# Kernel tuning notes

Measured on AMD Instinct MI355X. Metric: run time of the kernel, lower is better.

Reference implementation:

```python
import jax, jax.numpy as jnp
import numpy as np

N = 50000      # nodes
E = 800000     # edges (before self-loops)
IN = 128       # in_channels
HID = 64       # hidden_channels (= per-head dim, concat=False)
H = 4          # heads
OUT = 40       # out_channels
L = 4          # num_layers
LN_EPS = 1e-5


def setup_inputs() -> dict:
    key = jax.random.key(0)
    ks = jax.random.split(key, 12)
    s = 0.05
    return {
        "x": jax.random.normal(ks[0], (N, IN), jnp.float32),
        "edge_index": jax.random.randint(ks[1], (2, E), 0, N, dtype=jnp.int32),
        "Wi": jax.random.normal(ks[2], (IN, HID), jnp.float32) * s,
        "bi": jnp.zeros((HID,), jnp.float32),
        "lin_W": jax.random.normal(ks[3], (L, HID, H * HID), jnp.float32) * s,
        "att_src": jax.random.normal(ks[4], (L, H, HID), jnp.float32) * s,
        "att_dst": jax.random.normal(ks[5], (L, H, HID), jnp.float32) * s,
        "gat_b": jnp.zeros((L, HID), jnp.float32),
        "ln_g": jnp.ones((L, HID), jnp.float32),
        "ln_b": jnp.zeros((L, HID), jnp.float32),
        "Wo": jax.random.normal(ks[6], (HID, OUT), jnp.float32) * s,
        "bo": jnp.zeros((OUT,), jnp.float32),
    }


def _layer_norm(x, g, b):
    mu = jnp.mean(x, axis=-1, keepdims=True)
    var = jnp.mean(jnp.square(x - mu), axis=-1, keepdims=True)
    return (x - mu) * jax.lax.rsqrt(var + LN_EPS) * g + b


def _gat_conv(x, src, dst, W, a_src, a_dst, bias):
    # PyG GATConv: heads=H, out_channels=HID, concat=False (mean over heads),
    # negative_slope=0.2, self-loops already appended to (src, dst).
    xl = (x @ W).reshape(N, H, HID)                    # [N,H,C]
    alpha_s = jnp.einsum('nhc,hc->nh', xl, a_src)      # [N,H]
    alpha_d = jnp.einsum('nhc,hc->nh', xl, a_dst)      # [N,H]
    e = jax.nn.leaky_relu(alpha_s[src] + alpha_d[dst], 0.2)  # [Etot,H]
    # segment softmax over incoming edges of each destination node
    m = jax.ops.segment_max(e, dst, num_segments=N)    # [N,H]
    e = jnp.exp(e - m[dst])
    denom = jax.ops.segment_sum(e, dst, num_segments=N)
    alpha = e / (denom[dst] + 1e-16)                   # [Etot,H]
    msg = alpha[:, :, None] * xl[src]                  # [Etot,H,C]
    out = jax.ops.segment_sum(msg, dst, num_segments=N)  # [N,H,C]
    return out.mean(axis=1) + bias                     # concat=False -> mean


def reference(x, edge_index, Wi, bi, lin_W, att_src, att_dst, gat_b, ln_g, ln_b, Wo, bo):
    # add self-loops (GATConv default add_self_loops=True)
    loops = jnp.arange(N, dtype=edge_index.dtype)
    src = jnp.concatenate([edge_index[0], loops])
    dst = jnp.concatenate([edge_index[1], loops])

    h = jax.nn.elu(x @ Wi + bi)
    for i in range(L):
        residual = h
        h = _gat_conv(h, src, dst, lin_W[i], att_src[i], att_dst[i], gat_b[i])
        h = _layer_norm(h, ln_g[i], ln_b[i])
        h = jax.nn.elu(h)
        if i > 0:
            h = h + residual
        # dropout p=0.0 -> identity
    return h @ Wo + bo
```

## Files before the change

kernel.cpp:

```cpp
#include <hip/hip_runtime.h>
#include <hip/hip_bf16.h>

#define N_NODES 50000
#define N_EDGES 800000
#define E_TOT   (N_EDGES + N_NODES)
#define IN_CH   128
#define HID     64
#define HEADS   4
#define OUT_CH  40
#define LAYERS  4
#define LN_EPS  1e-5f

#define AG_STRIDE  262
#define WC_STRIDE  68

__device__ __forceinline__ unsigned short f2bf(float f) {
    unsigned u = __float_as_uint(f);
    unsigned r = (u + 0x7fffu + ((u >> 16) & 1u)) >> 16;
    return (unsigned short)r;
}
__device__ __forceinline__ float bf_lo(unsigned u) { return __uint_as_float(u << 16); }
__device__ __forceinline__ float bf_hi(unsigned u) { return __uint_as_float(u & 0xffff0000u); }
__device__ __forceinline__ float lrelu(float x) { return x > 0.f ? x : 0.2f * x; }

__device__ __forceinline__ unsigned fenc(float f) {
    unsigned u = __float_as_uint(f);
    return (u & 0x80000000u) ? ~u : (u | 0x80000000u);
}
__device__ __forceinline__ float fdec(unsigned k) {
    unsigned u = (k & 0x80000000u) ? (k & 0x7fffffffu) : ~k;
    return __uint_as_float(u);
}


__global__ void k_hist(const int* __restrict__ ei, int* __restrict__ cnt,
                       int* __restrict__ rank) {
    int e = blockIdx.x * blockDim.x + threadIdx.x;
    if (e >= E_TOT) return;
    int dst = (e < N_EDGES) ? ei[N_EDGES + e] : (e - N_EDGES);
    rank[e] = atomicAdd(&cnt[dst], 1);
}

__global__ __launch_bounds__(1024) void k_scan_a(const int* __restrict__ cnt,
                                                 int* __restrict__ row_ptr,
                                                 int* __restrict__ bsum) {
    __shared__ int wt[16];
    int tid = threadIdx.x, lane = tid & 63, w = tid >> 6;
    int i = blockIdx.x * 1024 + tid;
    int v = (i < N_NODES) ? cnt[i] : 0;
    int x = v;
    for (int off = 1; off < 64; off <<= 1) {
        int t = __shfl_up(x, off, 64);
        if (lane >= off) x += t;
    }
    if (lane == 63) wt[w] = x;
    __syncthreads();
    if (w == 0) {
        int t = (lane < 16) ? wt[lane] : 0;
        for (int off = 1; off < 16; off <<= 1) {
            int u = __shfl_up(t, off, 64);
            if (lane >= off) t += u;
        }
        if (lane < 16) wt[lane] = t;
    }
    __syncthreads();
    int woff = (w > 0) ? wt[w - 1] : 0;
    if (i < N_NODES) row_ptr[i] = woff + x - v;
    if (tid == 0) bsum[blockIdx.x] = wt[15];
}

#define SCAN_BLOCKS 49

__global__ __launch_bounds__(64) void k_scan_b(const int* __restrict__ bsum,
                                               int* __restrict__ boff,
                                               int* __restrict__ row_ptr) {
    int lane = threadIdx.x;
    int v = (lane < SCAN_BLOCKS) ? bsum[lane] : 0;
    int x = v;
    for (int off = 1; off < 64; off <<= 1) {
        int t = __shfl_up(x, off, 64);
        if (lane >= off) x += t;
    }
    if (lane < SCAN_BLOCKS) boff[lane] = x - v;
    if (lane == 63) row_ptr[N_NODES] = x;
}

__global__ __launch_bounds__(256) void k_scan_c(int* __restrict__ row_ptr,
                                                const int* __restrict__ boff) {
    int i = blockIdx.x * 256 + threadIdx.x;
    if (i >= N_NODES) return;
    row_ptr[i] += boff[i >> 10];
}

__global__ void k_scatter(const int* __restrict__ ei,
                          const int* __restrict__ row_ptr,
                          const int* __restrict__ rank,
                          int* __restrict__ csr_src) {
    int e = blockIdx.x * blockDim.x + threadIdx.x;
    if (e >= E_TOT) return;
    int src, dst;
    if (e < N_EDGES) { src = ei[e]; dst = ei[N_EDGES + e]; }
    else             { src = dst = e - N_EDGES; }
    int pos = row_ptr[dst] + rank[e];
    csr_src[pos] = src;
}


__global__ __launch_bounds__(256) void k_prep(const float* __restrict__ lin_W,
                                              const float* __restrict__ att_src,
                                              const float* __restrict__ att_dst,
                                              float* __restrict__ watt,
                                              float* __restrict__ wstack) {
    int l = blockIdx.x, tid = threadIdx.x;
    const float* Wl = lin_W + (size_t)l * HID * 256;
    {
        int k = tid, h = k >> 6, i = k & 63;
        const float* src = Wl + i * 256 + h * 64;
        float* dstp = wstack + (size_t)l * 256 * 64 + k * 64;
        for (int c = 0; c < 64; c += 4)
            *(float4*)(dstp + c) = *(const float4*)(src + c);
    }
    for (int idx = tid; idx < 512; idx += 256) {
        int v = idx >> 6, i = idx & 63;
        int h = v & 3;
        const float* av = (v < 4 ? att_src : att_dst) + (size_t)l * 256 + h * 64;
        const float* wr = Wl + i * 256 + h * 64;
        float p = 0.f;
        for (int c = 0; c < 64; ++c) p = fmaf(wr[c], av[c], p);
        watt[(size_t)l * 512 + v * 64 + i] = p;
    }
}


__global__ __launch_bounds__(256) void k_gemm_in(const float* __restrict__ x,
                                                 const float* __restrict__ Wi,
                                                 const float* __restrict__ bi,
                                                 const float* __restrict__ watt,
                                                 float* __restrict__ h,
                                                 unsigned short* __restrict__ h_bf,
                                                 float* __restrict__ alpha_s,
                                                 float* __restrict__ alpha_d,
                                                 unsigned* __restrict__ mxk) {
    __shared__ float xT[IN_CH * 64];
    __shared__ float Ws[IN_CH * HID];
    __shared__ float wl[512];
    __shared__ unsigned s_mx[4];
    int tid = threadIdx.x;
    int row0 = blockIdx.x * 64;
    if (tid < 4) s_mx[tid] = 0;
    for (int i = tid; i < 512; i += 256) wl[i] = watt[i];
    for (int i = tid * 4; i < IN_CH * HID; i += 1024)
        *(float4*)(Ws + i) = *(const float4*)(Wi + i);
    {
        int r = tid >> 2, k0 = (tid & 3) * 32;
        int rr = row0 + r;
#pragma unroll
        for (int j = 0; j < 32; j += 4) {
            float4 v = (rr < N_NODES) ? *(const float4*)(x + (size_t)rr * IN_CH + k0 + j)
                                      : make_float4(0.f, 0.f, 0.f, 0.f);
            xT[(k0 + j    ) * 64 + r] = v.x;
            xT[(k0 + j + 1) * 64 + r] = v.y;
            xT[(k0 + j + 2) * 64 + r] = v.z;
            xT[(k0 + j + 3) * 64 + r] = v.w;
        }
    }
    __syncthreads();
    int tx = tid & 15, ty = tid >> 4;
    int c0 = tx * 4, r0 = ty * 4;
    float acc[4][4] = {};
    for (int k = 0; k < IN_CH; ++k) {
        float4 xv = *(const float4*)(xT + k * 64 + r0);
        float4 wv = *(const float4*)(Ws + k * HID + c0);
        float xr[4] = {xv.x, xv.y, xv.z, xv.w};
        float wc[4] = {wv.x, wv.y, wv.z, wv.w};
#pragma unroll
        for (int r = 0; r < 4; ++r)
#pragma unroll
            for (int c = 0; c < 4; ++c)
                acc[r][c] = fmaf(xr[r], wc[c], acc[r][c]);
    }
    float4 bv = *(const float4*)(bi + c0);
    float bcs[4] = {bv.x, bv.y, bv.z, bv.w};
    float rpmax[4] = {-1e30f, -1e30f, -1e30f, -1e30f};
#pragma unroll
    for (int r = 0; r < 4; ++r) {
        int rr = row0 + r0 + r;
        float vv[4];
#pragma unroll
        for (int c = 0; c < 4; ++c) {
            float t = acc[r][c] + bcs[c];
            vv[c] = t > 0.f ? t : (__expf(t) - 1.f);
        }
        if (rr < N_NODES) {
            *(float4*)(h + (size_t)rr * HID + c0) = make_float4(vv[0], vv[1], vv[2], vv[3]);
            unsigned short t4[4] = {f2bf(vv[0]), f2bf(vv[1]), f2bf(vv[2]), f2bf(vv[3])};
            *(uint2*)(h_bf + (size_t)rr * HID + c0) = *(uint2*)t4;
        }
        float red[8];
#pragma unroll
        for (int v = 0; v < 8; ++v) {
            const float* wv = wl + v * 64 + c0;
            float p = vv[0]*wv[0] + vv[1]*wv[1] + vv[2]*wv[2] + vv[3]*wv[3];
            p += __shfl_xor(p, 1, 64);
            p += __shfl_xor(p, 2, 64);
            p += __shfl_xor(p, 4, 64);
            p += __shfl_xor(p, 8, 64);
            red[v] = p;
        }
        if (tx == 0 && rr < N_NODES) {
            *(float4*)(alpha_s + (size_t)rr * 4) = make_float4(red[0], red[1], red[2], red[3]);
            *(float4*)(alpha_d + (size_t)rr * 4) = make_float4(red[4], red[5], red[6], red[7]);
#pragma unroll
            for (int hh = 0; hh < 4; ++hh) rpmax[hh] = fmaxf(rpmax[hh], red[hh]);
        }
    }
    if (tx == 0) {
#pragma unroll
        for (int hh = 0; hh < 4; ++hh) atomicMax(&s_mx[hh], fenc(rpmax[hh]));
    }
    __syncthreads();
    if (tid < 4) atomicMax(&mxk[tid], s_mx[tid]);
}


__global__ __launch_bounds__(256) void k_layer(
    const unsigned short* __restrict__ h_bf,
    const float* __restrict__ alpha_s,
    const float* __restrict__ alpha_d,
    const int* __restrict__ row_ptr,
    const int* __restrict__ csr_src,
    const unsigned* __restrict__ mxk,
    const float* __restrict__ wstack,
    const float* __restrict__ gat_b,
    const float* __restrict__ ln_g,
    const float* __restrict__ ln_b,
    const float* __restrict__ h_res,
    const float* __restrict__ watt_next,
    float* __restrict__ h_out,
    unsigned short* __restrict__ hbf_out,
    float* __restrict__ alpha_s_nxt,
    float* __restrict__ alpha_d_nxt,
    unsigned* __restrict__ mxk_next,
    int use_res, int do_alpha)
{
    __shared__ unsigned short aS[32 * AG_STRIDE];
    __shared__ float Wc[32 * WC_STRIDE];
    __shared__ unsigned s_mx[4];
    int tid = threadIdx.x;
    int row0 = blockIdx.x * 32;
    if (tid < 4) s_mx[tid] = 0;

    {
        int dl = tid >> 3, q = tid & 7;
        int d = row0 + dl;
        unsigned short* arow = aS + dl * AG_STRIDE + (q << 3);
        if (d < N_NODES) {
            int start = row_ptr[d], end = row_ptr[d + 1];
            float4 ad = *(const float4*)(alpha_d + (size_t)d * 4);
            float mp0 = lrelu(fdec(mxk[0]) + ad.x);
            float mp1 = lrelu(fdec(mxk[1]) + ad.y);
            float mp2 = lrelu(fdec(mxk[2]) + ad.z);
            float mp3 = lrelu(fdec(mxk[3]) + ad.w);

            float acc[4][8] = {};
            float ds0 = 0.f, ds1 = 0.f, ds2 = 0.f, ds3 = 0.f;

            int s = csr_src[start];
            float4 as = *(const float4*)(alpha_s + (size_t)s * 4);
            uint4  u  = *(const uint4*)(h_bf + ((size_t)s << 6) + (q << 3));

            for (int e = start; e < end; ++e) {
                int sn = (e + 1 < end) ? csr_src[e + 1] : 0;
                float4 as_n = *(const float4*)(alpha_s + (size_t)sn * 4);
                uint4  u_n  = *(const uint4*)(h_bf + ((size_t)sn << 6) + (q << 3));

                float w0 = __expf(lrelu(as.x + ad.x) - mp0);
                float w1 = __expf(lrelu(as.y + ad.y) - mp1);
                float w2 = __expf(lrelu(as.z + ad.z) - mp2);
                float w3 = __expf(lrelu(as.w + ad.w) - mp3);
                ds0 += w0; ds1 += w1; ds2 += w2; ds3 += w3;
                float f0 = bf_lo(u.x), f1 = bf_hi(u.x), f2 = bf_lo(u.y), f3 = bf_hi(u.y);
                float f4 = bf_lo(u.z), f5 = bf_hi(u.z), f6 = bf_lo(u.w), f7 = bf_hi(u.w);
                acc[0][0] = fmaf(w0, f0, acc[0][0]); acc[0][1] = fmaf(w0, f1, acc[0][1]);
                acc[0][2] = fmaf(w0, f2, acc[0][2]); acc[0][3] = fmaf(w0, f3, acc[0][3]);
                acc[0][4] = fmaf(w0, f4, acc[0][4]); acc[0][5] = fmaf(w0, f5, acc[0][5]);
                acc[0][6] = fmaf(w0, f6, acc[0][6]); acc[0][7] = fmaf(w0, f7, acc[0][7]);
                acc[1][0] = fmaf(w1, f0, acc[1][0]); acc[1][1] = fmaf(w1, f1, acc[1][1]);
                acc[1][2] = fmaf(w1, f2, acc[1][2]); acc[1][3] = fmaf(w1, f3, acc[1][3]);
                acc[1][4] = fmaf(w1, f4, acc[1][4]); acc[1][5] = fmaf(w1, f5, acc[1][5]);
                acc[1][6] = fmaf(w1, f6, acc[1][6]); acc[1][7] = fmaf(w1, f7, acc[1][7]);
                acc[2][0] = fmaf(w2, f0, acc[2][0]); acc[2][1] = fmaf(w2, f1, acc[2][1]);
                acc[2][2] = fmaf(w2, f2, acc[2][2]); acc[2][3] = fmaf(w2, f3, acc[2][3]);
                acc[2][4] = fmaf(w2, f4, acc[2][4]); acc[2][5] = fmaf(w2, f5, acc[2][5]);
                acc[2][6] = fmaf(w2, f6, acc[2][6]); acc[2][7] = fmaf(w2, f7, acc[2][7]);
                acc[3][0] = fmaf(w3, f0, acc[3][0]); acc[3][1] = fmaf(w3, f1, acc[3][1]);
                acc[3][2] = fmaf(w3, f2, acc[3][2]); acc[3][3] = fmaf(w3, f3, acc[3][3]);
                acc[3][4] = fmaf(w3, f4, acc[3][4]); acc[3][5] = fmaf(w3, f5, acc[3][5]);
                acc[3][6] = fmaf(w3, f6, acc[3][6]); acc[3][7] = fmaf(w3, f7, acc[3][7]);

                as = as_n; u = u_n; s = sn;
            }

            float inv[4] = {1.f / (ds0 + 1e-16f), 1.f / (ds1 + 1e-16f),
                            1.f / (ds2 + 1e-16f), 1.f / (ds3 + 1e-16f)};
#pragma unroll
            for (int hh = 0; hh < 4; ++hh) {
                unsigned short t8[8];
#pragma unroll
                for (int k = 0; k < 8; ++k) t8[k] = f2bf(acc[hh][k] * inv[hh]);
                *(uint4*)(arow + hh * 64) = *(uint4*)t8;
            }
        } else {
            uint4 z = make_uint4(0, 0, 0, 0);
#pragma unroll
            for (int hh = 0; hh < 4; ++hh) *(uint4*)(arow + hh * 64) = z;
        }
    }

    int tx = tid & 15, ty = tid >> 4;
    int c0 = tx * 4, r0 = ty * 2;
    float acc[2][4] = {};

    int wk = tid >> 3;
    int wc8 = (tid & 7) * 8;
    for (int chunk = 0; chunk < 8; ++chunk) {
        __syncthreads();
        {
            const float* wsrc = wstack + (size_t)(chunk * 32 + wk) * 64 + wc8;
            float* wdst = Wc + wk * WC_STRIDE + wc8;
            *(float4*)(wdst)     = *(const float4*)(wsrc);
            *(float4*)(wdst + 4) = *(const float4*)(wsrc + 4);
        }
        __syncthreads();
        int kbase = chunk * 32;
#pragma unroll
        for (int kb = 0; kb < 8; ++kb) {
            int kl = kb * 4;
            float4 w0 = *(const float4*)(Wc + (kl + 0) * WC_STRIDE + c0);
            float4 w1 = *(const float4*)(Wc + (kl + 1) * WC_STRIDE + c0);
            float4 w2 = *(const float4*)(Wc + (kl + 2) * WC_STRIDE + c0);
            float4 w3 = *(const float4*)(Wc + (kl + 3) * WC_STRIDE + c0);
#pragma unroll
            for (int r = 0; r < 2; ++r) {
                uint2 au = *(const uint2*)(aS + (r0 + r) * AG_STRIDE + kbase + kl);
                float a0 = bf_lo(au.x), a1 = bf_hi(au.x), a2 = bf_lo(au.y), a3 = bf_hi(au.y);
                acc[r][0] = fmaf(a0, w0.x, fmaf(a1, w1.x, fmaf(a2, w2.x, fmaf(a3, w3.x, acc[r][0]))));
                acc[r][1] = fmaf(a0, w0.y, fmaf(a1, w1.y, fmaf(a2, w2.y, fmaf(a3, w3.y, acc[r][1]))));
                acc[r][2] = fmaf(a0, w0.z, fmaf(a1, w1.z, fmaf(a2, w2.z, fmaf(a3, w3.z, acc[r][2]))));
                acc[r][3] = fmaf(a0, w0.w, fmaf(a1, w1.w, fmaf(a2, w2.w, fmaf(a3, w3.w, acc[r][3]))));
            }
        }
    }

    float4 gb = *(const float4*)(gat_b + c0);
    float bias[4] = {gb.x, gb.y, gb.z, gb.w};
    float4 lg = *(const float4*)(ln_g + c0);
    float4 lb = *(const float4*)(ln_b + c0);
    float gg[4] = {lg.x, lg.y, lg.z, lg.w};
    float bb[4] = {lb.x, lb.y, lb.z, lb.w};
    float rpmax[4] = {-1e30f, -1e30f, -1e30f, -1e30f};
#pragma unroll
    for (int r = 0; r < 2; ++r) {
        int rr = row0 + r0 + r;
        float o[4];
#pragma unroll
        for (int c = 0; c < 4; ++c) o[c] = acc[r][c] * 0.25f + bias[c];
        float s = o[0] + o[1] + o[2] + o[3];
        float s2 = o[0]*o[0] + o[1]*o[1] + o[2]*o[2] + o[3]*o[3];
        for (int off = 1; off < 16; off <<= 1) {
            s  += __shfl_xor(s,  off, 64);
            s2 += __shfl_xor(s2, off, 64);
        }
        float mu = s * (1.f / 64.f);
        float var = s2 * (1.f / 64.f) - mu * mu;
        float rstd = rsqrtf(var + LN_EPS);
        float vv[4];
#pragma unroll
        for (int c = 0; c < 4; ++c) {
            float t = (o[c] - mu) * rstd * gg[c] + bb[c];
            vv[c] = t > 0.f ? t : (__expf(t) - 1.f);
        }
        if (rr < N_NODES) {
            if (use_res) {
                float4 rv = *(const float4*)(h_res + (size_t)rr * HID + c0);
                vv[0] += rv.x; vv[1] += rv.y; vv[2] += rv.z; vv[3] += rv.w;
            }
            *(float4*)(h_out + (size_t)rr * HID + c0) = make_float4(vv[0], vv[1], vv[2], vv[3]);
            unsigned short t4[4] = {f2bf(vv[0]), f2bf(vv[1]), f2bf(vv[2]), f2bf(vv[3])};
            *(uint2*)(hbf_out + (size_t)rr * HID + c0) = *(uint2*)t4;
        }
        if (do_alpha) {
            float red[8];
#pragma unroll
            for (int v = 0; v < 8; ++v) {
                const float* wv = watt_next + v * 64 + c0;
                float p = vv[0]*wv[0] + vv[1]*wv[1] + vv[2]*wv[2] + vv[3]*wv[3];
                p += __shfl_xor(p, 1, 64);
                p += __shfl_xor(p, 2, 64);
                p += __shfl_xor(p, 4, 64);
                p += __shfl_xor(p, 8, 64);
                red[v] = p;
            }
            if (tx == 0 && rr < N_NODES) {
                *(float4*)(alpha_s_nxt + (size_t)rr * 4) = make_float4(red[0], red[1], red[2], red[3]);
                *(float4*)(alpha_d_nxt + (size_t)rr * 4) = make_float4(red[4], red[5], red[6], red[7]);
#pragma unroll
                for (int hh = 0; hh < 4; ++hh) rpmax[hh] = fmaxf(rpmax[hh], red[hh]);
            }
        }
    }
    if (do_alpha) {
        if (tx == 0) {
#pragma unroll
            for (int hh = 0; hh < 4; ++hh) atomicMax(&s_mx[hh], fenc(rpmax[hh]));
        }
        __syncthreads();
        if (tid < 4) atomicMax(&mxk_next[tid], s_mx[tid]);
    }
}


__global__ __launch_bounds__(256) void k_gemm_out(const float* __restrict__ h,
                                                  const float* __restrict__ Wo,
                                                  const float* __restrict__ bo,
                                                  float* __restrict__ out) {
    __shared__ float Ws[HID * OUT_CH];
    __shared__ float hs[6 * HID];
    int tid = threadIdx.x;
    int row0 = blockIdx.x * 6;
    for (int i = tid; i < HID * OUT_CH; i += 256) Ws[i] = Wo[i];
    for (int i = tid; i < 6 * HID; i += 256) {
        int r = row0 + (i >> 6);
        hs[i] = (r < N_NODES) ? h[(size_t)r * HID + (i & 63)] : 0.f;
    }
    __syncthreads();
    if (tid < 240) {
        int r = tid / 40, o = tid - r * 40;
        int rr = row0 + r;
        if (rr < N_NODES) {
            float acc = bo[o];
            for (int k = 0; k < HID; ++k)
                acc = fmaf(hs[r * HID + k], Ws[k * OUT_CH + o], acc);
            out[(size_t)row0 * OUT_CH + tid] = acc;
        }
    }
}


extern "C" void kernel_launch(void* const* d_in, const int* in_sizes, int n_in,
                              void* d_out, int out_size, void* d_ws, size_t ws_size,
                              hipStream_t stream) {
    const float* x       = (const float*)d_in[0];
    const int*   ei      = (const int*)  d_in[1];
    const float* Wi      = (const float*)d_in[2];
    const float* bi      = (const float*)d_in[3];
    const float* lin_W   = (const float*)d_in[4];
    const float* att_src = (const float*)d_in[5];
    const float* att_dst = (const float*)d_in[6];
    const float* gat_b   = (const float*)d_in[7];
    const float* ln_g    = (const float*)d_in[8];
    const float* ln_b    = (const float*)d_in[9];
    const float* Wo      = (const float*)d_in[10];
    const float* bo      = (const float*)d_in[11];
    float* out = (float*)d_out;

    char* ws = (char*)d_ws;
    size_t off = 0;
    auto alloc = [&](size_t bytes) -> void* {
        void* p = ws + off;
        off += (bytes + 255) & ~(size_t)255;
        return p;
    };
    float*          h_a      = (float*)alloc((size_t)N_NODES * HID * 4);
    float*          h_b      = (float*)alloc((size_t)N_NODES * HID * 4);
    unsigned short* hbf_a    = (unsigned short*)alloc((size_t)N_NODES * HID * 2);
    unsigned short* hbf_b    = (unsigned short*)alloc((size_t)N_NODES * HID * 2);
    float*          als_a    = (float*)alloc((size_t)N_NODES * 4 * 4);
    float*          ald_a    = (float*)alloc((size_t)N_NODES * 4 * 4);
    float*          als_b    = (float*)alloc((size_t)N_NODES * 4 * 4);
    float*          ald_b    = (float*)alloc((size_t)N_NODES * 4 * 4);
    int*            cnt      = (int*)  alloc((size_t)N_NODES * 4);
    int*            row_ptr  = (int*)  alloc((size_t)(N_NODES + 1) * 4);
    int*            csr_src  = (int*)  alloc((size_t)E_TOT * 4);
    int*            rank     = (int*)  alloc((size_t)E_TOT * 4);
    unsigned*       maxkey   = (unsigned*)alloc((size_t)LAYERS * 4 * 4);
    int*            bsum     = (int*)  alloc((size_t)SCAN_BLOCKS * 4);
    int*            boff     = (int*)  alloc((size_t)SCAN_BLOCKS * 4);
    float*          watt     = (float*)alloc((size_t)LAYERS * 8 * 64 * 4);
    float*          wstack   = (float*)alloc((size_t)LAYERS * 256 * 64 * 4);

    hipMemsetAsync(cnt, 0, (size_t)N_NODES * 4, stream);
    hipMemsetAsync(maxkey, 0, (size_t)LAYERS * 4 * 4, stream);

    int egrid = (E_TOT + 255) / 256;
    k_hist<<<egrid, 256, 0, stream>>>(ei, cnt, rank);
    k_scan_a<<<SCAN_BLOCKS, 1024, 0, stream>>>(cnt, row_ptr, bsum);
    k_scan_b<<<1, 64, 0, stream>>>(bsum, boff, row_ptr);
    k_scan_c<<<(N_NODES + 255) / 256, 256, 0, stream>>>(row_ptr, boff);
    k_scatter<<<egrid, 256, 0, stream>>>(ei, row_ptr, rank, csr_src);

    k_prep<<<LAYERS, 256, 0, stream>>>(lin_W, att_src, att_dst, watt, wstack);

    int rtiles = (N_NODES + 63) / 64;
    k_gemm_in<<<rtiles, 256, 0, stream>>>(x, Wi, bi, watt, h_a, hbf_a,
                                          als_a, ald_a, maxkey);

    int lgrid = (N_NODES + 31) / 32;
    float*          h_cur   = h_a;   float*          h_nxt   = h_b;
    unsigned short* hbf_cur = hbf_a; unsigned short* hbf_nxt = hbf_b;
    float* als_cur = als_a; float* ald_cur = ald_a;
    float* als_nxt = als_b; float* ald_nxt = ald_b;
    for (int l = 0; l < LAYERS; ++l) {
        int do_alpha = (l + 1 < LAYERS) ? 1 : 0;
        k_layer<<<lgrid, 256, 0, stream>>>(hbf_cur, als_cur, ald_cur, row_ptr, csr_src,
                                           maxkey + l * 4,
                                           wstack + (size_t)l * 256 * 64,
                                           gat_b + (size_t)l * HID,
                                           ln_g + (size_t)l * HID,
                                           ln_b + (size_t)l * HID,
                                           h_cur,
                                           watt + (size_t)((l + 1) % LAYERS) * 512,
                                           h_nxt, hbf_nxt,
                                           als_nxt, ald_nxt,
                                           maxkey + (size_t)((l + 1) % LAYERS) * 4,
                                           l > 0 ? 1 : 0, do_alpha);
        { float* t = h_cur; h_cur = h_nxt; h_nxt = t; }
        { unsigned short* t = hbf_cur; hbf_cur = hbf_nxt; hbf_nxt = t; }
        { float* t = als_cur; als_cur = als_nxt; als_nxt = t; }
        { float* t = ald_cur; ald_cur = ald_nxt; ald_nxt = t; }
    }

    int ogrid = (N_NODES + 5) / 6;
    k_gemm_out<<<ogrid, 256, 0, stream>>>(h_cur, Wo, bo, out);
}
```

Baseline: 472.7 us.

## Reorder layer work by in-degree to balance per-block edge aggregation

Adds a counting sort of nodes by in-degree (descending, capped at 63) producing a permutation, and makes each layer kernel process nodes in that order so the 32 rows in a block have similar degrees. This reduces intra-block load imbalance, where threads wait on the highest-degree node of the tile. In exchange, output, residual and alpha writes become scattered through the permutation, and three small preprocessing kernels are added. The atomic-based scatter makes the order within each bucket nondeterministic.

```diff
diff --git a/kernel.cpp b/kernel.cpp
--- a/kernel.cpp
+++ b/kernel.cpp
@@ -103,6 +103,37 @@
     else             { src = dst = e - N_EDGES; }
     int pos = row_ptr[dst] + rank[e];
     csr_src[pos] = src;
+}
+
+
+__global__ __launch_bounds__(256) void k_dhist(const int* __restrict__ cnt,
+                                               int* __restrict__ dcnt) {
+    int i = blockIdx.x * 256 + threadIdx.x;
+    if (i >= N_NODES) return;
+    int b = min(cnt[i], 63);
+    atomicAdd(&dcnt[b], 1);
+}
+
+__global__ __launch_bounds__(64) void k_dscan(const int* __restrict__ dcnt,
+                                              int* __restrict__ dcur) {
+    int lane = threadIdx.x;
+    int v = dcnt[63 - lane];
+    int x = v;
+    for (int off = 1; off < 64; off <<= 1) {
+        int t = __shfl_up(x, off, 64);
+        if (lane >= off) x += t;
+    }
+    dcur[63 - lane] = x - v;
+}
+
+__global__ __launch_bounds__(256) void k_dscatter(const int* __restrict__ cnt,
+                                                  int* __restrict__ dcur,
+                                                  int* __restrict__ perm) {
+    int i = blockIdx.x * 256 + threadIdx.x;
+    if (i >= N_NODES) return;
+    int b = min(cnt[i], 63);
+    int pos = atomicAdd(&dcur[b], 1);
+    perm[pos] = i;
 }
 
 
@@ -229,6 +260,7 @@
     const float* __restrict__ alpha_d,
     const int* __restrict__ row_ptr,
     const int* __restrict__ csr_src,
+    const int* __restrict__ perm,
     const unsigned* __restrict__ mxk,
     const float* __restrict__ wstack,
     const float* __restrict__ gat_b,
@@ -252,9 +284,10 @@
 
     {
         int dl = tid >> 3, q = tid & 7;
-        int d = row0 + dl;
+        int idx = row0 + dl;
         unsigned short* arow = aS + dl * AG_STRIDE + (q << 3);
-        if (d < N_NODES) {
+        if (idx < N_NODES) {
+            int d = perm[idx];
             int start = row_ptr[d], end = row_ptr[d + 1];
             float4 ad = *(const float4*)(alpha_d + (size_t)d * 4);
             float mp0 = lrelu(fdec(mxk[0]) + ad.x);
@@ -361,7 +394,7 @@
     float rpmax[4] = {-1e30f, -1e30f, -1e30f, -1e30f};
 #pragma unroll
     for (int r = 0; r < 2; ++r) {
-        int rr = row0 + r0 + r;
+        int idx = row0 + r0 + r;
         float o[4];
 #pragma unroll
         for (int c = 0; c < 4; ++c) o[c] = acc[r][c] * 0.25f + bias[c];
@@ -380,14 +413,15 @@
             float t = (o[c] - mu) * rstd * gg[c] + bb[c];
             vv[c] = t > 0.f ? t : (__expf(t) - 1.f);
         }
-        if (rr < N_NODES) {
+        int node = (idx < N_NODES) ? perm[idx] : 0;
+        if (idx < N_NODES) {
             if (use_res) {
-                float4 rv = *(const float4*)(h_res + (size_t)rr * HID + c0);
+                float4 rv = *(const float4*)(h_res + (size_t)node * HID + c0);
                 vv[0] += rv.x; vv[1] += rv.y; vv[2] += rv.z; vv[3] += rv.w;
             }
-            *(float4*)(h_out + (size_t)rr * HID + c0) = make_float4(vv[0], vv[1], vv[2], vv[3]);
+            *(float4*)(h_out + (size_t)node * HID + c0) = make_float4(vv[0], vv[1], vv[2], vv[3]);
             unsigned short t4[4] = {f2bf(vv[0]), f2bf(vv[1]), f2bf(vv[2]), f2bf(vv[3])};
-            *(uint2*)(hbf_out + (size_t)rr * HID + c0) = *(uint2*)t4;
+            *(uint2*)(hbf_out + (size_t)node * HID + c0) = *(uint2*)t4;
         }
         if (do_alpha) {
             float red[8];
@@ -401,9 +435,9 @@
                 p += __shfl_xor(p, 8, 64);
                 red[v] = p;
             }
-            if (tx == 0 && rr < N_NODES) {
-                *(float4*)(alpha_s_nxt + (size_t)rr * 4) = make_float4(red[0], red[1], red[2], red[3]);
-                *(float4*)(alpha_d_nxt + (size_t)rr * 4) = make_float4(red[4], red[5], red[6], red[7]);
+            if (tx == 0 && idx < N_NODES) {
+                *(float4*)(alpha_s_nxt + (size_t)node * 4) = make_float4(red[0], red[1], red[2], red[3]);
+                *(float4*)(alpha_d_nxt + (size_t)node * 4) = make_float4(red[4], red[5], red[6], red[7]);
 #pragma unroll
                 for (int hh = 0; hh < 4; ++hh) rpmax[hh] = fmaxf(rpmax[hh], red[hh]);
             }
@@ -483,6 +517,9 @@
     int*            row_ptr  = (int*)  alloc((size_t)(N_NODES + 1) * 4);
     int*            csr_src  = (int*)  alloc((size_t)E_TOT * 4);
     int*            rank     = (int*)  alloc((size_t)E_TOT * 4);
+    int*            perm     = (int*)  alloc((size_t)N_NODES * 4);
+    int*            dcnt     = (int*)  alloc((size_t)64 * 4);
+    int*            dcur     = (int*)  alloc((size_t)64 * 4);
     unsigned*       maxkey   = (unsigned*)alloc((size_t)LAYERS * 4 * 4);
     int*            bsum     = (int*)  alloc((size_t)SCAN_BLOCKS * 4);
     int*            boff     = (int*)  alloc((size_t)SCAN_BLOCKS * 4);
@@ -490,14 +527,19 @@
     float*          wstack   = (float*)alloc((size_t)LAYERS * 256 * 64 * 4);
 
     hipMemsetAsync(cnt, 0, (size_t)N_NODES * 4, stream);
+    hipMemsetAsync(dcnt, 0, (size_t)64 * 4, stream);
     hipMemsetAsync(maxkey, 0, (size_t)LAYERS * 4 * 4, stream);
 
     int egrid = (E_TOT + 255) / 256;
+    int ngrid = (N_NODES + 255) / 256;
     k_hist<<<egrid, 256, 0, stream>>>(ei, cnt, rank);
     k_scan_a<<<SCAN_BLOCKS, 1024, 0, stream>>>(cnt, row_ptr, bsum);
     k_scan_b<<<1, 64, 0, stream>>>(bsum, boff, row_ptr);
-    k_scan_c<<<(N_NODES + 255) / 256, 256, 0, stream>>>(row_ptr, boff);
+    k_scan_c<<<ngrid, 256, 0, stream>>>(row_ptr, boff);
     k_scatter<<<egrid, 256, 0, stream>>>(ei, row_ptr, rank, csr_src);
+    k_dhist<<<ngrid, 256, 0, stream>>>(cnt, dcnt);
+    k_dscan<<<1, 64, 0, stream>>>(dcnt, dcur);
+    k_dscatter<<<ngrid, 256, 0, stream>>>(cnt, dcur, perm);
 
     k_prep<<<LAYERS, 256, 0, stream>>>(lin_W, att_src, att_dst, watt, wstack);
 
@@ -512,7 +554,7 @@
     float* als_nxt = als_b; float* ald_nxt = ald_b;
     for (int l = 0; l < LAYERS; ++l) {
         int do_alpha = (l + 1 < LAYERS) ? 1 : 0;
-        k_layer<<<lgrid, 256, 0, stream>>>(hbf_cur, als_cur, ald_cur, row_ptr, csr_src,
+        k_layer<<<lgrid, 256, 0, stream>>>(hbf_cur, als_cur, ald_cur, row_ptr, csr_src, perm,
                                            maxkey + l * 4,
                                            wstack + (size_t)l * 256 * 64,
                                            gat_b + (size_t)l * HID,
```

New measurement: 732.2 us. 1.55x slower.
